# Optimization experiments

Hardware: AMD Instinct MI355X
Metric: run time of the kernel (lower is better)

## Reference

```python
import jax, jax.numpy as jnp
import numpy as np
import math

B, N, D = 4, 4096, 1024
H = 16
HD = D // H  # 64
R = 256      # num random features
EPS = 1e-6


def _orthogonal_random_matrix(num_rows, num_cols, rng):
    """Blocks of orthogonal matrices (QR of Gaussian), row-scaled to sqrt(num_cols)."""
    blocks = []
    for _ in range(num_rows // num_cols + 1):
        g = rng.standard_normal((num_cols, num_cols)).astype(np.float32)
        q, _ = np.linalg.qr(g)
        blocks.append(q.T)
    raw = np.concatenate(blocks, axis=0)[:num_rows]
    scaling = math.sqrt(num_cols)
    raw = raw * (scaling / (np.linalg.norm(raw, axis=1, keepdims=True) + 1e-8))
    return jnp.asarray(raw, dtype=jnp.float32)


def setup_inputs() -> dict:
    key = jax.random.key(0)
    k_x, k_qkv, k_proj, k_b = jax.random.split(key, 4)
    rng = np.random.default_rng(0)
    x = jax.random.normal(k_x, (B, N, D), dtype=jnp.float32)
    # nn.Linear weights, stored as (in, out) for x @ W
    w_qkv = jax.random.normal(k_qkv, (D, 3 * D), dtype=jnp.float32) / math.sqrt(D)
    w_proj = jax.random.normal(k_proj, (D, D), dtype=jnp.float32) / math.sqrt(D)
    b_proj = jax.random.normal(k_b, (D,), dtype=jnp.float32) * 0.01
    projection = _orthogonal_random_matrix(R, HD, rng)  # (R, HD)
    return {"x": x, "w_qkv": w_qkv, "w_proj": w_proj, "b_proj": b_proj,
            "projection": projection}


def _favor_map(x, projection):
    # x: (B,H,N,d), projection: (r,d) -> phi(x): (B,H,N,r), softmax kernel
    projected = jnp.einsum('bhnd,rd->bhnr', x, projection)
    x_norm_sq = jnp.sum(x * x, axis=-1, keepdims=True) * 0.5
    feat = jnp.exp(projected - x_norm_sq) / math.sqrt(projection.shape[0])
    return feat + EPS


def reference(x, w_qkv, w_proj, b_proj, projection):
    # qkv projection: (B,N,3D) -> (3,B,H,N,d)
    qkv = x @ w_qkv
    qkv = qkv.reshape(B, N, 3, H, HD).transpose(2, 0, 3, 1, 4)
    q, k, v = qkv[0], qkv[1], qkv[2]
    q_feat = _favor_map(q, projection)  # (B,H,N,r)
    k_feat = _favor_map(k, projection)  # (B,H,N,r)
    kv = jnp.einsum('bhnr,bhnd->bhrd', k_feat, v)        # (B,H,r,d)
    out = jnp.einsum('bhnr,bhrd->bhnd', q_feat, kv)      # (B,H,N,d)
    k_sum = k_feat.sum(axis=2)                           # (B,H,r)
    denom = jnp.einsum('bhnr,bhr->bhn', q_feat, k_sum)   # (B,H,N)
    out = out / (denom[..., None] + EPS)
    out = out.transpose(0, 2, 1, 3).reshape(B, N, D)     # (B,N,D)
    return out @ w_proj + b_proj
```

## Files before the change

kernel.cpp:

```cpp
#include <hip/hip_runtime.h>

typedef unsigned short u16;
typedef unsigned int u32;
typedef __bf16 bf16x8 __attribute__((ext_vector_type(8)));
typedef float f32x4 __attribute__((ext_vector_type(4)));
typedef u32 u32x4 __attribute__((ext_vector_type(4)));

#define MFMA(a,b,c) __builtin_amdgcn_mfma_f32_16x16x32_bf16((a),(b),(c),0,0,0)

#define BB 4
#define NN 4096
#define DD 1024
#define HH 16
#define HDIM 64
#define RR 256
#define NBH 64
#define KSP 8

__device__ __forceinline__ float bf2f(u16 h){
  union { u32 u; float f; } c; c.u = ((u32)h) << 16; return c.f;
}
__device__ __forceinline__ u16 f2bf(float f){
  union { float f; u32 u; } c; c.f = f;
  u32 u = c.u;
  return (u16)((u + 0x7FFFu + ((u >> 16) & 1u)) >> 16);
}
__device__ __forceinline__ f32x4 zero4(){ f32x4 v = {0.f,0.f,0.f,0.f}; return v; }

__device__ __forceinline__ void gload16(const void* g, void* l) {
  __builtin_amdgcn_global_load_lds(
      (const __attribute__((address_space(1))) void*)g,
      (__attribute__((address_space(3))) void*)l, 16, 0, 0);
}


__global__ void split_cast_x2_kernel(const float4* __restrict__ src, u16* __restrict__ x2, int n4)
{
  int i = blockIdx.x * blockDim.x + threadIdx.x;
  int stride = gridDim.x * blockDim.x;
  for (; i < n4; i += stride) {
    float4 v = src[i];
    int m = i >> 8;
    int k4 = (i & 255) * 4;
    ushort4 h, lo;
    h.x = f2bf(v.x); lo.x = f2bf(v.x - bf2f(h.x));
    h.y = f2bf(v.y); lo.y = f2bf(v.y - bf2f(h.y));
    h.z = f2bf(v.z); lo.z = f2bf(v.z - bf2f(h.z));
    h.w = f2bf(v.w); lo.w = f2bf(v.w - bf2f(h.w));
    *(ushort4*)&x2[(size_t)m * 2048 + k4] = h;
    *(ushort4*)&x2[(size_t)m * 2048 + 1024 + k4] = lo;
  }
}

__global__ void split_cast_proj_kernel(const float4* __restrict__ src,
                                       ushort4* __restrict__ hi, ushort4* __restrict__ lo,
                                       u16* __restrict__ hia, u16* __restrict__ loa)
{
  int i = blockIdx.x * blockDim.x + threadIdx.x;
  if (i >= 4096) return;
  float4 v = src[i];
  ushort4 h, l4;
  h.x = f2bf(v.x); l4.x = f2bf(v.x - bf2f(h.x));
  h.y = f2bf(v.y); l4.y = f2bf(v.y - bf2f(h.y));
  h.z = f2bf(v.z); l4.z = f2bf(v.z - bf2f(h.z));
  h.w = f2bf(v.w); l4.w = f2bf(v.w - bf2f(h.w));
  hi[i] = h;
  lo[i] = l4;
  int prow = i >> 4;
  int c4 = (i & 15) * 4;
  int drow = (prow & ~31) | (((prow >> 2) & 3) << 3) | (((prow >> 4) & 1) << 2) | (prow & 3);
  *(ushort4*)&hia[drow * 64 + c4] = h;
  *(ushort4*)&loa[drow * 64 + c4] = l4;
}

__global__ void transpose_wqkv_kernel(const float* __restrict__ src,
                                      u16* __restrict__ w2qk, u16* __restrict__ wv)
{
  __shared__ float T[32][33];
  const int c0 = blockIdx.x * 32, r0 = blockIdx.y * 32;
  const int t = threadIdx.x;
  #pragma unroll
  for (int i = 0; i < 4; ++i) {
    int r = t >> 3, c = (t & 7) + i * 8;
    T[r][c] = src[(size_t)(r0 + r) * 3072 + c0 + c];
  }
  __syncthreads();
  #pragma unroll
  for (int i = 0; i < 4; ++i) {
    int r = t >> 3, c = (t & 7) + i * 8;
    float v = T[c][r];
    int orow = c0 + r, ocol = r0 + c;
    u16 h = f2bf(v);
    if (orow < 2048) {
      w2qk[(size_t)orow * 2048 + ocol] = h;
      w2qk[(size_t)orow * 2048 + 1024 + ocol] = h;
    } else {
      wv[(size_t)(orow - 2048) * 1024 + ocol] = h;
    }
  }
}

__global__ void transpose_kernel(const float* __restrict__ src, u16* __restrict__ dst)
{
  __shared__ float T[32][33];
  const int c0 = blockIdx.x * 32, r0 = blockIdx.y * 32;
  const int t = threadIdx.x;
  #pragma unroll
  for (int i = 0; i < 4; ++i) {
    int r = t >> 3, c = (t & 7) + i * 8;
    T[r][c] = src[(size_t)(r0 + r) * 1024 + c0 + c];
  }
  __syncthreads();
  #pragma unroll
  for (int i = 0; i < 4; ++i) {
    int r = t >> 3, c = (t & 7) + i * 8;
    dst[(size_t)(c0 + r) * 1024 + r0 + c] = f2bf(T[c][r]);
  }
}

template<int MODE>
__launch_bounds__(512, 2)
__global__ void gemm256_kernel(const u16* __restrict__ A, const u16* __restrict__ B,
                               const int K, const int lda, const int ldb,
                               u16* __restrict__ o0, u16* __restrict__ o1,
                               u16* __restrict__ o2, u16* __restrict__ o3,
                               float* __restrict__ fout, const float* __restrict__ bias)
{
  __shared__ __align__(16) u16 lds[2][2][256 * 64];
  const int t = threadIdx.x;
  const int w = t >> 6, l = t & 63;
  const int m0 = blockIdx.x * 256, n0 = blockIdx.y * 256;
  const int wm = w & 1, wn = w >> 1;
  const int lr = l & 15, lq = l >> 4;
  const int srow = l >> 3;
  const int gs = ((l & 7) ^ srow) * 8;
  const int swz = lr & 7;

  f32x4 acc[8][4];
  #pragma unroll
  for (int m = 0; m < 8; ++m)
    #pragma unroll
    for (int n = 0; n < 4; ++n) acc[m][n] = zero4();

  const int nt = K / 64;

  auto stage = [&](int kt, int bi) {
    #pragma unroll
    for (int i = 0; i < 4; ++i) {
      const int chunk = w * 4 + i;
      const int row = chunk * 8 + srow;
      gload16(&A[(size_t)(m0 + row) * lda + kt * 64 + gs],
              &lds[bi][0][chunk * 512 + l * 8]);
    }
    #pragma unroll
    for (int i = 0; i < 4; ++i) {
      const int chunk = w * 4 + i;
      const int row = chunk * 8 + srow;
      gload16(&B[(size_t)(n0 + row) * ldb + kt * 64 + gs],
              &lds[bi][1][chunk * 512 + l * 8]);
    }
  };

  stage(0, 0);
  stage(1, 1);
  asm volatile("s_waitcnt vmcnt(8)" ::: "memory");
  __builtin_amdgcn_s_barrier();
  __builtin_amdgcn_sched_barrier(0);

  for (int kt = 0; kt < nt; ++kt) {
    const int bi = kt & 1;
    const u16* la = &lds[bi][0][0];
    const u16* lb = &lds[bi][1][0];
    bf16x8 a0[8], b0[4], a1[8], b1[4];
    #pragma unroll
    for (int m = 0; m < 8; ++m)
      a0[m] = *(const bf16x8*)&la[(wm*128 + m*16 + lr)*64 + ((lq ^ swz) * 8)];
    #pragma unroll
    for (int n = 0; n < 4; ++n)
      b0[n] = *(const bf16x8*)&lb[(wn*64 + n*16 + lr)*64 + ((lq ^ swz) * 8)];
    __builtin_amdgcn_s_setprio(1);
    #pragma unroll
    for (int m = 0; m < 8; ++m)
      #pragma unroll
      for (int n = 0; n < 4; ++n)
        acc[m][n] = MFMA(a0[m], b0[n], acc[m][n]);
    __builtin_amdgcn_s_setprio(0);
    #pragma unroll
    for (int m = 0; m < 8; ++m)
      a1[m] = *(const bf16x8*)&la[(wm*128 + m*16 + lr)*64 + (((4 + lq) ^ swz) * 8)];
    #pragma unroll
    for (int n = 0; n < 4; ++n)
      b1[n] = *(const bf16x8*)&lb[(wn*64 + n*16 + lr)*64 + (((4 + lq) ^ swz) * 8)];
    asm volatile("s_waitcnt lgkmcnt(0)" ::: "memory");
    __builtin_amdgcn_s_barrier();
    __builtin_amdgcn_sched_barrier(0);
    if (kt + 2 < nt) stage(kt + 2, bi);
    __builtin_amdgcn_s_setprio(1);
    #pragma unroll
    for (int m = 0; m < 8; ++m)
      #pragma unroll
      for (int n = 0; n < 4; ++n)
        acc[m][n] = MFMA(a1[m], b1[n], acc[m][n]);
    __builtin_amdgcn_s_setprio(0);
    if (kt + 2 < nt)      { asm volatile("s_waitcnt vmcnt(8)" ::: "memory"); }
    else if (kt + 1 < nt) { asm volatile("s_waitcnt vmcnt(0)" ::: "memory"); }
    __builtin_amdgcn_s_barrier();
    __builtin_amdgcn_sched_barrier(0);
  }

  #pragma unroll
  for (int m = 0; m < 8; ++m)
    #pragma unroll
    for (int n = 0; n < 4; ++n)
      #pragma unroll
      for (int j = 0; j < 4; ++j) {
        int gm = m0 + wm*128 + m*16 + lq*4 + j;
        int gc = n0 + wn*64 + n*16 + lr;
        float v = acc[m][n][j];
        if (MODE == 2) {
          fout[(size_t)gm * 1024 + gc] = v + bias[gc];
        } else {
          int hh = (gc >> 6) & 15, hd = gc & 63;
          int b = gm >> 12, tok = gm & 4095;
          size_t idx = ((size_t)(b * HH + hh) * NN + tok) * HDIM + hd;
          if (MODE == 0) {
            u16 hi = f2bf(v), lo = f2bf(v - bf2f(hi));
            if ((gc >> 10) == 0) { o0[idx] = hi; o1[idx] = lo; }
            else                 { o2[idx] = hi; o3[idx] = lo; }
          } else {
            o0[idx] = f2bf(v);
          }
        }
      }
}

__launch_bounds__(256)
__global__ void k2a_kernel(const u16* __restrict__ khi, const u16* __restrict__ klo,
                           const u16* __restrict__ vb,
                           const u16* __restrict__ phi, const u16* __restrict__ plo,
                           float* __restrict__ kvpart)
{
  __shared__ __align__(16) u16 Kh[32*72];
  __shared__ __align__(16) u16 Kl[32*72];
  __shared__ __align__(16) u16 Kft[256*40];
  __shared__ __align__(16) u16 Vt[80*40];
  __shared__ float xnorm[32];
  const int bh = blockIdx.x, sp = blockIdx.y;
  const int t = threadIdx.x, w = t >> 6, l = t & 63;
  const int lr = l & 15, lk = (l >> 4) * 8, l4 = (l >> 4) * 4;
  const size_t base = (size_t)bh * NN * HDIM;
  f32x4 kvacc[4][5];
  #pragma unroll
  for (int i = 0; i < 4; ++i)
    #pragma unroll
    for (int j = 0; j < 5; ++j) kvacc[i][j] = zero4();

  const int TILES = (NN / KSP) / 32;
  for (int tile = 0; tile < TILES; ++tile) {
    const int nb = sp * (NN / KSP) + tile * 32;
    __syncthreads();
    {
      int row = t >> 3, c8 = (t & 7) * 8;
      size_t g = base + (size_t)(nb + row) * HDIM + c8;
      uint4 khv = *(const uint4*)&khi[g];
      uint4 klv = *(const uint4*)&klo[g];
      *(uint4*)&Kh[row*72 + c8] = khv;
      *(uint4*)&Kl[row*72 + c8] = klv;
      uint4 vv = *(const uint4*)&vb[g];
      const u16* pv = (const u16*)&vv;
      #pragma unroll
      for (int j = 0; j < 8; ++j) Vt[(c8 + j)*40 + row] = pv[j];
      if (t < 32) {
        Vt[64*40 + t] = 0x3F80u;
        #pragma unroll
        for (int d = 65; d < 80; ++d) Vt[d*40 + t] = 0;
      }
      const u16* ph = (const u16*)&khv;
      const u16* pl = (const u16*)&klv;
      float s = 0.f;
      #pragma unroll
      for (int j = 0; j < 8; ++j) {
        float qv = bf2f(ph[j]) + bf2f(pl[j]);
        s += qv * qv;
      }
      s += __shfl_xor(s, 1);
      s += __shfl_xor(s, 2);
      s += __shfl_xor(s, 4);
      if ((t & 7) == 0) xnorm[row] = 0.5f * s;
    }
    __syncthreads();
    f32x4 facc[2][4];
    #pragma unroll
    for (int i = 0; i < 2; ++i)
      #pragma unroll
      for (int j = 0; j < 4; ++j) facc[i][j] = zero4();
    #pragma unroll
    for (int ks = 0; ks < 2; ++ks) {
      bf16x8 ah[2], al[2];
      #pragma unroll
      for (int fm = 0; fm < 2; ++fm) {
        ah[fm] = *(const bf16x8*)&Kh[(fm*16 + lr)*72 + ks*32 + lk];
        al[fm] = *(const bf16x8*)&Kl[(fm*16 + lr)*72 + ks*32 + lk];
      }
      #pragma unroll
      for (int fn = 0; fn < 4; ++fn) {
        int r = w*64 + fn*16 + lr;
        bf16x8 pbh = *(const bf16x8*)&phi[r*HDIM + ks*32 + lk];
        bf16x8 pbl = *(const bf16x8*)&plo[r*HDIM + ks*32 + lk];
        #pragma unroll
        for (int fm = 0; fm < 2; ++fm) {
          facc[fm][fn] = MFMA(al[fm], pbh, facc[fm][fn]);
          facc[fm][fn] = MFMA(ah[fm], pbl, facc[fm][fn]);
          facc[fm][fn] = MFMA(ah[fm], pbh, facc[fm][fn]);
        }
      }
    }
    #pragma unroll
    for (int fm = 0; fm < 2; ++fm)
      #pragma unroll
      for (int fn = 0; fn < 4; ++fn)
        #pragma unroll
        for (int j = 0; j < 4; ++j) {
          int row = fm*16 + l4 + j;
          int r = w*64 + fn*16 + lr;
          float e = __expf(facc[fm][fn][j] - xnorm[row]) * 0.0625f + 1e-6f;
          Kft[r*40 + row] = f2bf(e);
        }
    __syncthreads();
    {
      bf16x8 bv[5];
      #pragma unroll
      for (int fn = 0; fn < 5; ++fn)
        bv[fn] = *(const bf16x8*)&Vt[(fn*16 + lr)*40 + lk];
      #pragma unroll
      for (int fr = 0; fr < 4; ++fr) {
        bf16x8 a = *(const bf16x8*)&Kft[(w*64 + fr*16 + lr)*40 + lk];
        #pragma unroll
        for (int fn = 0; fn < 5; ++fn) kvacc[fr][fn] = MFMA(a, bv[fn], kvacc[fr][fn]);
      }
    }
  }
  #pragma unroll
  for (int fr = 0; fr < 4; ++fr)
    #pragma unroll
    for (int fn = 0; fn < 5; ++fn)
      #pragma unroll
      for (int j = 0; j < 4; ++j) {
        int r = w*64 + fr*16 + l4 + j;
        int d = fn*16 + lr;
        kvpart[(((size_t)bh*KSP + sp)*80 + d)*256 + r] = kvacc[fr][fn][j];
      }
}

__global__ void kv_reduce_kernel(const float* __restrict__ kvpart, u16* __restrict__ kvt)
{
  int i = blockIdx.x * 256 + threadIdx.x;
  if (i >= NBH * 80 * 256) return;
  int bh = i / (80 * 256), rem = i - bh * (80 * 256);
  float s = 0.f;
  #pragma unroll
  for (int sp = 0; sp < KSP; ++sp)
    s += kvpart[((size_t)bh*KSP + sp)*80*256 + rem];
  kvt[i] = f2bf(s);
}

__launch_bounds__(512, 2)
__global__ void k2b_kernel(const u16* __restrict__ qhi, const u16* __restrict__ qlo,
                           const u16* __restrict__ kvt,
                           const u16* __restrict__ phi, const u16* __restrict__ plo,
                           u16* __restrict__ attn)
{
  __shared__ __align__(16) u16 KV[80*256];
  __shared__ __align__(16) u16 PH[256*64];
  __shared__ __align__(16) u16 PL[256*64];
  const int bh = blockIdx.x, b = bh >> 4, h = bh & 15;
  const int c0 = blockIdx.y * 512;
  const int t = threadIdx.x, w = t >> 6, l = t & 63;
  const int lr = l & 15, lq = l >> 4;
  const size_t base = (size_t)bh * NN * HDIM;

  {
    const uint4* kvg = (const uint4*)(kvt + (size_t)bh * 80 * 256);
    #pragma unroll
    for (int i = 0; i < 5; ++i) {
      int idx = t + i * 512;
      int d = idx >> 5, rb = idx & 31;
      *(uint4*)((char*)KV + d * 512 + ((rb ^ (d & 7)) << 4)) = kvg[idx];
    }
    const uint4* pg = (const uint4*)phi;
    const uint4* lg = (const uint4*)plo;
    #pragma unroll
    for (int i = 0; i < 4; ++i) {
      int idx = t + i * 512;
      int fr = idx >> 3, sl = idx & 7;
      int off = fr * 128 + (((sl ^ (fr & 7))) << 4);
      *(uint4*)((char*)PH + off) = pg[idx];
      *(uint4*)((char*)PL + off) = lg[idx];
    }
  }
  __syncthreads();

  const int swl = (lr & 7) << 4;
  #pragma unroll 1
  for (int tile = 0; tile < 4; ++tile) {
    const int r0 = c0 + tile * 128 + w * 16;
    bf16x8 ah0, ah1, al0, al1;
    {
      size_t g = base + (size_t)(r0 + lr) * HDIM + lq*8;
      ah0 = *(const bf16x8*)&qhi[g];
      al0 = *(const bf16x8*)&qlo[g];
      ah1 = *(const bf16x8*)&qhi[g + 32];
      al1 = *(const bf16x8*)&qlo[g + 32];
    }
    float s = 0.f;
    #pragma unroll
    for (int e = 0; e < 8; ++e) {
      float q0 = (float)ah0[e] + (float)al0[e];
      float q1 = (float)ah1[e] + (float)al1[e];
      s += q0 * q0 + q1 * q1;
    }
    s += __shfl_xor(s, 16);
    s += __shfl_xor(s, 32);
    const float xn = 0.5f * s;

    f32x4 oa0 = zero4(), oa1 = zero4(), oa2 = zero4(), oa3 = zero4(), oa4 = zero4();

    #pragma unroll 1
    for (int i = 0; i < 8; ++i) {
      f32x4 f0 = zero4(), f1 = zero4();
      {
        const int ro0 = (32*i + lr) * 128;
        const int ro1 = ro0 + 2048;
        const int cb0 = (lq*16) ^ swl;
        const int cb1 = (64 + lq*16) ^ swl;
        bf16x8 v;
        v = *(const bf16x8*)((const char*)PH + ro0 + cb0);
        f0 = MFMA(v, ah0, f0); f0 = MFMA(v, al0, f0);
        v = *(const bf16x8*)((const char*)PL + ro0 + cb0);
        f0 = MFMA(v, ah0, f0);
        v = *(const bf16x8*)((const char*)PH + ro0 + cb1);
        f0 = MFMA(v, ah1, f0); f0 = MFMA(v, al1, f0);
        v = *(const bf16x8*)((const char*)PL + ro0 + cb1);
        f0 = MFMA(v, ah1, f0);
        v = *(const bf16x8*)((const char*)PH + ro1 + cb0);
        f1 = MFMA(v, ah0, f1); f1 = MFMA(v, al0, f1);
        v = *(const bf16x8*)((const char*)PL + ro1 + cb0);
        f1 = MFMA(v, ah0, f1);
        v = *(const bf16x8*)((const char*)PH + ro1 + cb1);
        f1 = MFMA(v, ah1, f1); f1 = MFMA(v, al1, f1);
        v = *(const bf16x8*)((const char*)PL + ro1 + cb1);
        f1 = MFMA(v, ah1, f1);
      }
      u32x4 aw;
      aw.x = (u32)f2bf(__expf(f0[0] - xn) * 0.0625f + 1e-6f)
           | ((u32)f2bf(__expf(f0[1] - xn) * 0.0625f + 1e-6f) << 16);
      aw.y = (u32)f2bf(__expf(f0[2] - xn) * 0.0625f + 1e-6f)
           | ((u32)f2bf(__expf(f0[3] - xn) * 0.0625f + 1e-6f) << 16);
      aw.z = (u32)f2bf(__expf(f1[0] - xn) * 0.0625f + 1e-6f)
           | ((u32)f2bf(__expf(f1[1] - xn) * 0.0625f + 1e-6f) << 16);
      aw.w = (u32)f2bf(__expf(f1[2] - xn) * 0.0625f + 1e-6f)
           | ((u32)f2bf(__expf(f1[3] - xn) * 0.0625f + 1e-6f) << 16);
      bf16x8 a = __builtin_bit_cast(bf16x8, aw);
      const int kvsw = (((i << 2) | lq) ^ (lr & 7)) << 4;
      oa0 = MFMA(a, *(const bf16x8*)((const char*)KV + (0*16+lr)*512 + kvsw), oa0);
      oa1 = MFMA(a, *(const bf16x8*)((const char*)KV + (1*16+lr)*512 + kvsw), oa1);
      oa2 = MFMA(a, *(const bf16x8*)((const char*)KV + (2*16+lr)*512 + kvsw), oa2);
      oa3 = MFMA(a, *(const bf16x8*)((const char*)KV + (3*16+lr)*512 + kvsw), oa3);
      oa4 = MFMA(a, *(const bf16x8*)((const char*)KV + (4*16+lr)*512 + kvsw), oa4);
      __builtin_amdgcn_sched_barrier(0);
    }
    #pragma unroll
    for (int j = 0; j < 4; ++j) {
      float dn = __shfl(oa4[j], l & 48) + 1e-6f;
      float inv = 1.0f / dn;
      int q = r0 + lq*4 + j;
      u16* arow = attn + ((size_t)b * NN + q) * DD + h * HDIM + lr;
      arow[0]  = f2bf(oa0[j] * inv);
      arow[16] = f2bf(oa1[j] * inv);
      arow[32] = f2bf(oa2[j] * inv);
      arow[48] = f2bf(oa3[j] * inv);
    }
  }
}


extern "C" void kernel_launch(void* const* d_in, const int* in_sizes, int n_in,
                              void* d_out, int out_size, void* d_ws, size_t ws_size,
                              hipStream_t stream)
{
  const float* x      = (const float*)d_in[0];
  const float* w_qkv  = (const float*)d_in[1];
  const float* w_proj = (const float*)d_in[2];
  const float* b_proj = (const float*)d_in[3];
  const float* proj   = (const float*)d_in[4];
  float* out = (float*)d_out;

  char* p = (char*)d_ws;
  auto alloc = [&](size_t nbytes) {
    char* r = p; p += (nbytes + 255) & ~(size_t)255; return r;
  };
  const size_t NE = (size_t)16777216;
  u16* x2    = (u16*)alloc(NE * 2 * 2);
  u16* w2qk  = (u16*)alloc((size_t)2048 * 2048 * 2);
  u16* wv    = (u16*)alloc((size_t)1024 * 1024 * 2);
  u16* wpt   = (u16*)alloc((size_t)1024 * 1024 * 2);
  u16* phi   = (u16*)alloc((size_t)16384 * 2);
  u16* plo   = (u16*)alloc((size_t)16384 * 2);
  u16* phi_a = (u16*)alloc((size_t)16384 * 2);
  u16* plo_a = (u16*)alloc((size_t)16384 * 2);
  u16* qhi   = (u16*)alloc(NE * 2);
  u16* qlo   = (u16*)alloc(NE * 2);
  u16* khi   = (u16*)alloc(NE * 2);
  u16* klo   = (u16*)alloc(NE * 2);
  u16* vbuf  = (u16*)alloc(NE * 2);
  u16* kvt   = (u16*)alloc((size_t)NBH * 80 * 256 * 2);
  float* kvpart = (float*)x2;
  u16*   attn   = khi;

  split_cast_x2_kernel<<<2048, 256, 0, stream>>>((const float4*)x, x2, (int)(NE / 4));
  split_cast_proj_kernel<<<16, 256, 0, stream>>>(
      (const float4*)proj, (ushort4*)phi, (ushort4*)plo, phi_a, plo_a);
  transpose_wqkv_kernel<<<dim3(96, 32), 256, 0, stream>>>(w_qkv, w2qk, wv);
  transpose_kernel<<<dim3(32, 32), 256, 0, stream>>>(w_proj, wpt);

  gemm256_kernel<0><<<dim3(64, 8), 512, 0, stream>>>(
      x2, w2qk, 2048, 2048, 2048, qhi, qlo, khi, klo, nullptr, nullptr);
  gemm256_kernel<1><<<dim3(64, 4), 512, 0, stream>>>(
      x2, wv, 1024, 2048, 1024, vbuf, nullptr, nullptr, nullptr, nullptr, nullptr);

  k2a_kernel<<<dim3(64, KSP), 256, 0, stream>>>(khi, klo, vbuf, phi_a, plo_a, kvpart);
  kv_reduce_kernel<<<dim3(5120), 256, 0, stream>>>(kvpart, kvt);
  k2b_kernel<<<dim3(64, 8), 512, 0, stream>>>(qhi, qlo, kvt, phi, plo, attn);

  gemm256_kernel<2><<<dim3(64, 4), 512, 0, stream>>>(
      attn, wpt, 1024, 1024, 1024,
      nullptr, nullptr, nullptr, nullptr, out, b_proj);
}
```

Measured before the change: 349.3 us.

## Split GEMM LDS tiles into K-halves and interleave half-tile prefetch with MFMA

The 256x256 GEMM kernel now stores each K-tile as two 32-wide halves with a new 4-way XOR swizzle, and loads A fragments in groups of four instead of eight. LDS reads are interleaved with MFMA groups, and the next tile's global-to-LDS copy is issued in two halves at separate points in the iteration. The aim is to overlap LDS loads and global prefetch more finely with matrix math and to cut register pressure. The cost is more waitcnt and barrier points per iteration, and the new swizzle may cause different bank conflicts.

```diff
diff --git a/kernel.cpp b/kernel.cpp
--- a/kernel.cpp
+++ b/kernel.cpp
@@ -126,15 +126,12 @@
                                u16* __restrict__ o2, u16* __restrict__ o3,
                                float* __restrict__ fout, const float* __restrict__ bias)
 {
-  __shared__ __align__(16) u16 lds[2][2][256 * 64];
+  __shared__ __align__(16) char lds[131072];
   const int t = threadIdx.x;
   const int w = t >> 6, l = t & 63;
   const int m0 = blockIdx.x * 256, n0 = blockIdx.y * 256;
   const int wm = w & 1, wn = w >> 1;
   const int lr = l & 15, lq = l >> 4;
-  const int srow = l >> 3;
-  const int gs = ((l & 7) ^ srow) * 8;
-  const int swz = lr & 7;
 
   f32x4 acc[8][4];
   #pragma unroll
@@ -144,66 +141,100 @@
 
   const int nt = K / 64;
 
-  auto stage = [&](int kt, int bi) {
-    #pragma unroll
-    for (int i = 0; i < 4; ++i) {
-      const int chunk = w * 4 + i;
-      const int row = chunk * 8 + srow;
-      gload16(&A[(size_t)(m0 + row) * lda + kt * 64 + gs],
-              &lds[bi][0][chunk * 512 + l * 8]);
-    }
-    #pragma unroll
-    for (int i = 0; i < 4; ++i) {
-      const int chunk = w * 4 + i;
-      const int row = chunk * 8 + srow;
-      gload16(&B[(size_t)(n0 + row) * ldb + kt * 64 + gs],
-              &lds[bi][1][chunk * 512 + l * 8]);
+  auto stage_half = [&](int kt, int bi, int h) {
+    char* base = lds + bi * 65536 + h * 16384;
+    const int srow = l >> 2;
+    const int scol = kt * 64 + h * 32 + (((l & 3) ^ (srow & 3)) << 3);
+    #pragma unroll
+    for (int i = 0; i < 2; ++i) {
+      const int c = w * 2 + i;
+      gload16(&A[(size_t)(m0 + c * 16 + srow) * lda + scol], base + c * 1024 + l * 16);
+    }
+    #pragma unroll
+    for (int i = 0; i < 2; ++i) {
+      const int c = w * 2 + i;
+      gload16(&B[(size_t)(n0 + c * 16 + srow) * ldb + scol], base + 32768 + c * 1024 + l * 16);
     }
   };
 
-  stage(0, 0);
-  stage(1, 1);
+  stage_half(0, 0, 0); stage_half(0, 0, 1);
+  stage_half(1, 1, 0); stage_half(1, 1, 1);
   asm volatile("s_waitcnt vmcnt(8)" ::: "memory");
   __builtin_amdgcn_s_barrier();
   __builtin_amdgcn_sched_barrier(0);
 
   for (int kt = 0; kt < nt; ++kt) {
     const int bi = kt & 1;
-    const u16* la = &lds[bi][0][0];
-    const u16* lb = &lds[bi][1][0];
-    bf16x8 a0[8], b0[4], a1[8], b1[4];
-    #pragma unroll
-    for (int m = 0; m < 8; ++m)
-      a0[m] = *(const bf16x8*)&la[(wm*128 + m*16 + lr)*64 + ((lq ^ swz) * 8)];
+    const char* la = lds + bi * 65536;
+    const char* lb = la + 32768;
+    const int sw = (lq ^ (lr & 3)) << 4;
+    bf16x8 a0[4], a1[4], bb[4], b2[4];
+
+    #pragma unroll
+    for (int m = 0; m < 4; ++m)
+      a0[m] = *(const bf16x8*)(la + (wm*128 + m*16 + lr)*64 + sw);
     #pragma unroll
     for (int n = 0; n < 4; ++n)
-      b0[n] = *(const bf16x8*)&lb[(wn*64 + n*16 + lr)*64 + ((lq ^ swz) * 8)];
+      bb[n] = *(const bf16x8*)(lb + (wn*64 + n*16 + lr)*64 + sw);
+    asm volatile("s_waitcnt lgkmcnt(0)" ::: "memory");
+    __builtin_amdgcn_sched_barrier(0);
+    #pragma unroll
+    for (int m = 0; m < 4; ++m)
+      a1[m] = *(const bf16x8*)(la + (wm*128 + (m+4)*16 + lr)*64 + sw);
     __builtin_amdgcn_s_setprio(1);
     #pragma unroll
-    for (int m = 0; m < 8; ++m)
+    for (int m = 0; m < 4; ++m)
       #pragma unroll
       for (int n = 0; n < 4; ++n)
-        acc[m][n] = MFMA(a0[m], b0[n], acc[m][n]);
+        acc[m][n] = MFMA(a0[m], bb[n], acc[m][n]);
     __builtin_amdgcn_s_setprio(0);
-    #pragma unroll
-    for (int m = 0; m < 8; ++m)
-      a1[m] = *(const bf16x8*)&la[(wm*128 + m*16 + lr)*64 + (((4 + lq) ^ swz) * 8)];
+    asm volatile("s_waitcnt lgkmcnt(0)" ::: "memory");
+    __builtin_amdgcn_sched_barrier(0);
+    #pragma unroll
+    for (int m = 0; m < 4; ++m)
+      a0[m] = *(const bf16x8*)(la + 16384 + (wm*128 + m*16 + lr)*64 + sw);
     #pragma unroll
     for (int n = 0; n < 4; ++n)
-      b1[n] = *(const bf16x8*)&lb[(wn*64 + n*16 + lr)*64 + (((4 + lq) ^ swz) * 8)];
+      b2[n] = *(const bf16x8*)(lb + 16384 + (wn*64 + n*16 + lr)*64 + sw);
+    __builtin_amdgcn_s_setprio(1);
+    #pragma unroll
+    for (int m = 0; m < 4; ++m)
+      #pragma unroll
+      for (int n = 0; n < 4; ++n)
+        acc[m+4][n] = MFMA(a1[m], bb[n], acc[m+4][n]);
+    __builtin_amdgcn_s_setprio(0);
     asm volatile("s_waitcnt lgkmcnt(0)" ::: "memory");
+    __builtin_amdgcn_sched_barrier(0);
     __builtin_amdgcn_s_barrier();
     __builtin_amdgcn_sched_barrier(0);
-    if (kt + 2 < nt) stage(kt + 2, bi);
+    if (kt + 2 < nt) stage_half(kt + 2, bi, 0);
+    #pragma unroll
+    for (int m = 0; m < 4; ++m)
+      a1[m] = *(const bf16x8*)(la + 16384 + (wm*128 + (m+4)*16 + lr)*64 + sw);
     __builtin_amdgcn_s_setprio(1);
     #pragma unroll
-    for (int m = 0; m < 8; ++m)
+    for (int m = 0; m < 4; ++m)
       #pragma unroll
       for (int n = 0; n < 4; ++n)
-        acc[m][n] = MFMA(a1[m], b1[n], acc[m][n]);
+        acc[m][n] = MFMA(a0[m], b2[n], acc[m][n]);
     __builtin_amdgcn_s_setprio(0);
-    if (kt + 2 < nt)      { asm volatile("s_waitcnt vmcnt(8)" ::: "memory"); }
-    else if (kt + 1 < nt) { asm volatile("s_waitcnt vmcnt(0)" ::: "memory"); }
+    asm volatile("s_waitcnt lgkmcnt(0)" ::: "memory");
+    __builtin_amdgcn_sched_barrier(0);
+    __builtin_amdgcn_s_setprio(1);
+    #pragma unroll
+    for (int m = 0; m < 4; ++m)
+      #pragma unroll
+      for (int n = 0; n < 4; ++n)
+        acc[m+4][n] = MFMA(a1[m], b2[n], acc[m+4][n]);
+    __builtin_amdgcn_s_setprio(0);
+    __builtin_amdgcn_s_barrier();
+    __builtin_amdgcn_sched_barrier(0);
+    if (kt + 2 < nt) {
+      stage_half(kt + 2, bi, 1);
+      asm volatile("s_waitcnt vmcnt(8)" ::: "memory");
+    } else if (kt + 1 < nt) {
+      asm volatile("s_waitcnt vmcnt(0)" ::: "memory");
+    }
     __builtin_amdgcn_s_barrier();
     __builtin_amdgcn_sched_barrier(0);
   }
```

Measured after the change: 373.3 us. 1.07x slower.

## Feed K feature accumulators directly as MFMA operands, skipping LDS round-trip

Applied to the files above, without the earlier changes.

In the kv accumulation kernel, the exp'd random-feature values now stay in registers and are packed straight into the A operand of the second MFMA. V rows are permuted in shared memory so their order matches the accumulator layout. This drops the Kft shared buffer and one barrier per tile. Projection fragments are also loaded once into registers before the tile loop instead of being reloaded from global every tile. The cost is higher register pressure from the hoisted projection fragments, and correctness depends on the row permutation matching the MFMA output layout.

```diff
diff --git a/kernel.cpp b/kernel.cpp
--- a/kernel.cpp
+++ b/kernel.cpp
@@ -242,13 +242,23 @@
 {
   __shared__ __align__(16) u16 Kh[32*72];
   __shared__ __align__(16) u16 Kl[32*72];
-  __shared__ __align__(16) u16 Kft[256*40];
   __shared__ __align__(16) u16 Vt[80*40];
   __shared__ float xnorm[32];
   const int bh = blockIdx.x, sp = blockIdx.y;
   const int t = threadIdx.x, w = t >> 6, l = t & 63;
   const int lr = l & 15, lk = (l >> 4) * 8, l4 = (l >> 4) * 4;
   const size_t base = (size_t)bh * NN * HDIM;
+
+  bf16x8 pbh[4][2], pbl[4][2];
+  #pragma unroll
+  for (int fn = 0; fn < 4; ++fn)
+    #pragma unroll
+    for (int ks = 0; ks < 2; ++ks) {
+      int r = w*64 + fn*16 + lr;
+      pbh[fn][ks] = *(const bf16x8*)&phi[r*HDIM + ks*32 + lk];
+      pbl[fn][ks] = *(const bf16x8*)&plo[r*HDIM + ks*32 + lk];
+    }
+
   f32x4 kvacc[4][5];
   #pragma unroll
   for (int i = 0; i < 4; ++i)
@@ -256,6 +266,7 @@
     for (int j = 0; j < 5; ++j) kvacc[i][j] = zero4();
 
   const int TILES = (NN / KSP) / 32;
+  #pragma unroll 1
   for (int tile = 0; tile < TILES; ++tile) {
     const int nb = sp * (NN / KSP) + tile * 32;
     __syncthreads();
@@ -268,8 +279,9 @@
       *(uint4*)&Kl[row*72 + c8] = klv;
       uint4 vv = *(const uint4*)&vb[g];
       const u16* pv = (const u16*)&vv;
-      #pragma unroll
-      for (int j = 0; j < 8; ++j) Vt[(c8 + j)*40 + row] = pv[j];
+      int srow = ((row >> 2) & 3) * 8 + ((row >> 4) & 1) * 4 + (row & 3);
+      #pragma unroll
+      for (int j = 0; j < 8; ++j) Vt[(c8 + j)*40 + srow] = pv[j];
       if (t < 32) {
         Vt[64*40 + t] = 0x3F80u;
         #pragma unroll
@@ -303,52 +315,50 @@
         al[fm] = *(const bf16x8*)&Kl[(fm*16 + lr)*72 + ks*32 + lk];
       }
       #pragma unroll
-      for (int fn = 0; fn < 4; ++fn) {
-        int r = w*64 + fn*16 + lr;
-        bf16x8 pbh = *(const bf16x8*)&phi[r*HDIM + ks*32 + lk];
-        bf16x8 pbl = *(const bf16x8*)&plo[r*HDIM + ks*32 + lk];
+      for (int fn = 0; fn < 4; ++fn)
         #pragma unroll
         for (int fm = 0; fm < 2; ++fm) {
-          facc[fm][fn] = MFMA(al[fm], pbh, facc[fm][fn]);
-          facc[fm][fn] = MFMA(ah[fm], pbl, facc[fm][fn]);
-          facc[fm][fn] = MFMA(ah[fm], pbh, facc[fm][fn]);
+          facc[fm][fn] = MFMA(al[fm], pbh[fn][ks], facc[fm][fn]);
+          facc[fm][fn] = MFMA(ah[fm], pbl[fn][ks], facc[fm][fn]);
+          facc[fm][fn] = MFMA(ah[fm], pbh[fn][ks], facc[fm][fn]);
         }
-      }
-    }
+    }
+    float xb[2][4];
     #pragma unroll
     for (int fm = 0; fm < 2; ++fm)
       #pragma unroll
-      for (int fn = 0; fn < 4; ++fn)
-        #pragma unroll
-        for (int j = 0; j < 4; ++j) {
-          int row = fm*16 + l4 + j;
-          int r = w*64 + fn*16 + lr;
-          float e = __expf(facc[fm][fn][j] - xnorm[row]) * 0.0625f + 1e-6f;
-          Kft[r*40 + row] = f2bf(e);
-        }
-    __syncthreads();
-    {
-      bf16x8 bv[5];
-      #pragma unroll
-      for (int fn = 0; fn < 5; ++fn)
-        bv[fn] = *(const bf16x8*)&Vt[(fn*16 + lr)*40 + lk];
-      #pragma unroll
-      for (int fr = 0; fr < 4; ++fr) {
-        bf16x8 a = *(const bf16x8*)&Kft[(w*64 + fr*16 + lr)*40 + lk];
-        #pragma unroll
-        for (int fn = 0; fn < 5; ++fn) kvacc[fr][fn] = MFMA(a, bv[fn], kvacc[fr][fn]);
-      }
-    }
-  }
-  #pragma unroll
-  for (int fr = 0; fr < 4; ++fr)
-    #pragma unroll
-    for (int fn = 0; fn < 5; ++fn)
+      for (int j = 0; j < 4; ++j)
+        xb[fm][j] = xnorm[fm*16 + l4 + j];
+    bf16x8 bv[5];
+    #pragma unroll
+    for (int dn = 0; dn < 5; ++dn)
+      bv[dn] = *(const bf16x8*)&Vt[(dn*16 + lr)*40 + lk];
+    #pragma unroll
+    for (int fn = 0; fn < 4; ++fn) {
+      u32x4 aw;
+      aw.x = (u32)f2bf(__expf(facc[0][fn][0] - xb[0][0]) * 0.0625f + 1e-6f)
+           | ((u32)f2bf(__expf(facc[0][fn][1] - xb[0][1]) * 0.0625f + 1e-6f) << 16);
+      aw.y = (u32)f2bf(__expf(facc[0][fn][2] - xb[0][2]) * 0.0625f + 1e-6f)
+           | ((u32)f2bf(__expf(facc[0][fn][3] - xb[0][3]) * 0.0625f + 1e-6f) << 16);
+      aw.z = (u32)f2bf(__expf(facc[1][fn][0] - xb[1][0]) * 0.0625f + 1e-6f)
+           | ((u32)f2bf(__expf(facc[1][fn][1] - xb[1][1]) * 0.0625f + 1e-6f) << 16);
+      aw.w = (u32)f2bf(__expf(facc[1][fn][2] - xb[1][2]) * 0.0625f + 1e-6f)
+           | ((u32)f2bf(__expf(facc[1][fn][3] - xb[1][3]) * 0.0625f + 1e-6f) << 16);
+      bf16x8 a = __builtin_bit_cast(bf16x8, aw);
+      #pragma unroll
+      for (int dn = 0; dn < 5; ++dn)
+        kvacc[fn][dn] = MFMA(a, bv[dn], kvacc[fn][dn]);
+    }
+  }
+  #pragma unroll
+  for (int fn = 0; fn < 4; ++fn)
+    #pragma unroll
+    for (int dn = 0; dn < 5; ++dn)
       #pragma unroll
       for (int j = 0; j < 4; ++j) {
-        int r = w*64 + fr*16 + l4 + j;
-        int d = fn*16 + lr;
-        kvpart[(((size_t)bh*KSP + sp)*80 + d)*256 + r] = kvacc[fr][fn][j];
+        int r = w*64 + fn*16 + l4 + j;
+        int d = dn*16 + lr;
+        kvpart[(((size_t)bh*KSP + sp)*80 + d)*256 + r] = kvacc[fn][dn][j];
       }
 }
 
```

Measured after the change: 379.1 us. 1.09x slower.
